# Kernel tuning notes

Hardware: AMD Instinct MI355X
Metric: run time of the kernel (lower is better)

Reference implementation:

```python
import jax, jax.numpy as jnp
import numpy as np

HEAD_DIM = 128
SCALE = 1.0 / np.sqrt(HEAD_DIM)  # standard 1/sqrt(d) attention scaling


def setup_inputs() -> dict:
    key = jax.random.key(0)
    kq, kk, kv = jax.random.split(key, 3)
    q = jax.random.normal(kq, (2, 32, 2048, HEAD_DIM), dtype=jnp.float16)
    k = jax.random.normal(kk, (2, 8, 2048, HEAD_DIM), dtype=jnp.float16)
    v = jax.random.normal(kv, (2, 8, 2048, HEAD_DIM), dtype=jnp.float16)
    return {"q": q, "k": k, "v": v}


def reference(q, k, v):
    # GQA attention: each of the g = H // KVH query heads in a group attends
    # against the group's single shared K/V head (no K/V duplication).
    b, h, sq, d = q.shape
    kvh = k.shape[1]
    g = h // kvh
    # [b, kvh, g, sq, d] -- group-packed Q, mirroring the kernel's _pack_q
    qg = q.reshape(b, kvh, g, sq, d)
    # fp32 accumulation as in flash-attention kernels
    scores = jnp.einsum(
        'bhgqd,bhkd->bhgqk',
        qg.astype(jnp.float32), k.astype(jnp.float32)) * SCALE
    p = jax.nn.softmax(scores, axis=-1)  # non-causal, full attention
    o = jnp.einsum('bhgqk,bhkd->bhgqd', p, v.astype(jnp.float32))
    return o.reshape(b, h, sq, d).astype(q.dtype)
```

## Files before the change

### kernel.cpp

```cpp
#include <hip/hip_runtime.h>

#define SEQ   2048
#define HD    128
#define BN    64
#define NITER (SEQ / BN)

typedef __fp16 f16x8  __attribute__((ext_vector_type(8)));
typedef float  f32x4  __attribute__((ext_vector_type(4)));
typedef float  f32x16 __attribute__((ext_vector_type(16)));

__device__ __forceinline__ unsigned pkh(float a, float b) {
  auto h = __builtin_amdgcn_cvt_pkrtz(a, b);
  return __builtin_bit_cast(unsigned, h);
}

__global__ __launch_bounds__(256, 2)
void fa_gqa_kernel(const float* __restrict__ Q,
                   const float* __restrict__ K,
                   const float* __restrict__ V,
                   float* __restrict__ O)
{
  __shared__ unsigned short kt_lds[64 * HD];
  __shared__ unsigned short vt_lds[HD * 64];

  const int tid  = threadIdx.x;
  const int lane = tid & 63;
  const int w    = tid >> 6;
  const int ml   = lane & 31;
  const int hi   = lane >> 5;
  const bool hib = (hi != 0);

  const int F     = blockIdx.x;
  const int xcd   = F & 7;
  const int s     = F >> 3;
  const int bh    = xcd * 8 + (s >> 4);
  const int qtile = s & 15;

  const int b = bh >> 5;
  const int h = bh & 31;
  const long qrow0 = (long)bh * SEQ + qtile * 128 + w * 32;
  const float* Qw = Q + qrow0 * HD;
  float*       Ow = O + qrow0 * HD;
  const long kvoff = (long)(b * 8 + (h >> 2)) * SEQ * HD;
  const float* Kb = K + kvoff;
  const float* Vb = V + kvoff;

  f16x8 qf[8];
#pragma unroll
  for (int dc = 0; dc < 8; ++dc) {
    const float4* qp = (const float4*)(Qw + ml * HD + dc * 16 + hi * 8);
    float4 a = qp[0], bq = qp[1];
    int4 t;
    t.x = (int)pkh(a.x, a.y);
    t.y = (int)pkh(a.z, a.w);
    t.z = (int)pkh(bq.x, bq.y);
    t.w = (int)pkh(bq.z, bq.w);
    qf[dc] = __builtin_bit_cast(f16x8, t);
  }

  f32x16 oacc[4];
#pragma unroll
  for (int dt = 0; dt < 4; ++dt)
    oacc[dt] = (f32x16)(0.f);

  float mst = -1e30f;
  float lst = 0.f;

  const float K1 = 0.08838834764831845f * 1.4426950408889634f;

  const int krow = tid >> 2;
  const int kq4  = tid & 3;
  const int kq   = tid >> 4;
  const int dc8  = tid & 15;

  for (int it = 0; it < NITER; ++it) {
    const int k0 = it * BN;

    const float* kp = Kb + (long)(k0 + krow) * HD + kq4 * 32;
    int4 ks[4];
#pragma unroll
    for (int jj = 0; jj < 4; ++jj) {
      float4 e = ((const float4*)kp)[2 * jj];
      float4 o = ((const float4*)kp)[2 * jj + 1];
      ks[jj].x = (int)pkh(e.x, e.y);
      ks[jj].y = (int)pkh(e.z, e.w);
      ks[jj].z = (int)pkh(o.x, o.y);
      ks[jj].w = (int)pkh(o.z, o.w);
    }

    const float* vp = Vb + (long)(k0 + 4 * kq) * HD + dc8 * 8;
    float4 vr[4][2];
#pragma unroll
    for (int r = 0; r < 4; ++r) {
      vr[r][0] = ((const float4*)(vp + r * HD))[0];
      vr[r][1] = ((const float4*)(vp + r * HD))[1];
    }
    uint2 vs[8];
#pragma unroll
    for (int jd = 0; jd < 8; ++jd) {
      const int hsel = jd >> 2, e = jd & 3;
      float x0 = ((const float*)&vr[0][hsel])[e];
      float x1 = ((const float*)&vr[1][hsel])[e];
      float x2 = ((const float*)&vr[2][hsel])[e];
      float x3 = ((const float*)&vr[3][hsel])[e];
      vs[jd].x = pkh(x0, x1);
      vs[jd].y = pkh(x2, x3);
    }

    __syncthreads();

#pragma unroll
    for (int jj = 0; jj < 4; ++jj) {
      int j = kq4 * 4 + jj;
      int pos = j ^ (krow & 15);
      *(int4*)(kt_lds + krow * HD + pos * 8) = ks[jj];
    }
#pragma unroll
    for (int jd = 0; jd < 8; ++jd) {
      int d = dc8 * 8 + jd;
      int sw3 = ((d >> 3) ^ d) & 7;
      int pos = (kq >> 1) ^ sw3;
      *(uint2*)(vt_lds + d * 64 + pos * 8 + (kq & 1) * 4) = vs[jd];
    }

    __syncthreads();

    f32x16 sacc[2];
    sacc[0] = (f32x16)(0.f);
    sacc[1] = (f32x16)(0.f);

    __builtin_amdgcn_s_setprio(1);
#pragma unroll
    for (int dc = 0; dc < 8; ++dc) {
#pragma unroll
      for (int kt = 0; kt < 2; ++kt) {
        int row = kt * 32 + ml;
        int pos = (2 * dc + hi) ^ (row & 15);
        f16x8 af = *(const f16x8*)(kt_lds + row * HD + pos * 8);
        sacc[kt] = __builtin_amdgcn_mfma_f32_32x32x16_f16(
            af, qf[dc], sacc[kt], 0, 0, 0);
      }
    }
    __builtin_amdgcn_s_setprio(0);

    float x0 = fmaxf(sacc[0][0], sacc[1][0]);
    float x1 = fmaxf(sacc[0][1], sacc[1][1]);
    float x2 = fmaxf(sacc[0][2], sacc[1][2]);
    float x3 = fmaxf(sacc[0][3], sacc[1][3]);
#pragma unroll
    for (int r = 4; r < 16; r += 4) {
      x0 = fmaxf(x0, fmaxf(sacc[0][r + 0], sacc[1][r + 0]));
      x1 = fmaxf(x1, fmaxf(sacc[0][r + 1], sacc[1][r + 1]));
      x2 = fmaxf(x2, fmaxf(sacc[0][r + 2], sacc[1][r + 2]));
      x3 = fmaxf(x3, fmaxf(sacc[0][r + 3], sacc[1][r + 3]));
    }
    float mx = fmaxf(fmaxf(x0, x1), fmaxf(x2, x3));
    mx = fmaxf(mx, __shfl_xor(mx, 32, 64));

    if (__any(mx > mst)) {
      float mnew = fmaxf(mst, mx);
      float alpha = __builtin_amdgcn_exp2f(K1 * (mst - mnew));
      mst = mnew;
      lst *= alpha;
#pragma unroll
      for (int dt = 0; dt < 4; ++dt)
        oacc[dt] *= alpha;
    }

    const float nm = -K1 * mst;
    float p0 = 0.f, p1 = 0.f, p2 = 0.f, p3 = 0.f;
#pragma unroll
    for (int kt = 0; kt < 2; ++kt) {
#pragma unroll
      for (int r = 0; r < 16; r += 4) {
        float e0 = __builtin_amdgcn_exp2f(fmaf(sacc[kt][r + 0], K1, nm));
        float e1 = __builtin_amdgcn_exp2f(fmaf(sacc[kt][r + 1], K1, nm));
        float e2 = __builtin_amdgcn_exp2f(fmaf(sacc[kt][r + 2], K1, nm));
        float e3 = __builtin_amdgcn_exp2f(fmaf(sacc[kt][r + 3], K1, nm));
        sacc[kt][r + 0] = e0; p0 += e0;
        sacc[kt][r + 1] = e1; p1 += e1;
        sacc[kt][r + 2] = e2; p2 += e2;
        sacc[kt][r + 3] = e3; p3 += e3;
      }
    }
    lst += (p0 + p1) + (p2 + p3);

#pragma unroll
    for (int st = 0; st < 4; ++st) {
      const int kt = st >> 1;
      const int R  = 8 * (st & 1);
      unsigned pA0 = pkh(sacc[kt][R + 0], sacc[kt][R + 1]);
      unsigned pA1 = pkh(sacc[kt][R + 2], sacc[kt][R + 3]);
      unsigned pB0 = pkh(sacc[kt][R + 4], sacc[kt][R + 5]);
      unsigned pB1 = pkh(sacc[kt][R + 6], sacc[kt][R + 7]);
      unsigned s0 = hib ? pA0 : pB0;
      unsigned s1 = hib ? pA1 : pB1;
      unsigned r0 = (unsigned)__shfl_xor((int)s0, 32, 64);
      unsigned r1 = (unsigned)__shfl_xor((int)s1, 32, 64);
      int4 bf;
      bf.x = (int)(hib ? r0 : pA0);
      bf.y = (int)(hib ? r1 : pA1);
      bf.z = (int)(hib ? pB0 : r0);
      bf.w = (int)(hib ? pB1 : r1);
      f16x8 pfrag = __builtin_bit_cast(f16x8, bf);
      __builtin_amdgcn_s_setprio(1);
#pragma unroll
      for (int dt = 0; dt < 4; ++dt) {
        int d = dt * 32 + ml;
        int pos = (2 * st + hi) ^ (((d >> 3) ^ d) & 7);
        f16x8 vf = *(const f16x8*)(vt_lds + d * 64 + pos * 8);
        oacc[dt] = __builtin_amdgcn_mfma_f32_32x32x16_f16(
            vf, pfrag, oacc[dt], 0, 0, 0);
      }
      __builtin_amdgcn_s_setprio(0);
    }
  }

  float lf = lst + __shfl_xor(lst, 32, 64);
  float linv = 1.0f / lf;
#pragma unroll
  for (int dt = 0; dt < 4; ++dt) {
#pragma unroll
    for (int t = 0; t < 4; ++t) {
      f32x4 ov;
      ov[0] = oacc[dt][4 * t + 0] * linv;
      ov[1] = oacc[dt][4 * t + 1] * linv;
      ov[2] = oacc[dt][4 * t + 2] * linv;
      ov[3] = oacc[dt][4 * t + 3] * linv;
      *(f32x4*)(Ow + ml * HD + dt * 32 + 8 * t + 4 * hi) = ov;
    }
  }
}

extern "C" void kernel_launch(void* const* d_in, const int* in_sizes, int n_in,
                              void* d_out, int out_size, void* d_ws, size_t ws_size,
                              hipStream_t stream) {
  const float* q = (const float*)d_in[0];
  const float* k = (const float*)d_in[1];
  const float* v = (const float*)d_in[2];
  float* o = (float*)d_out;
  fa_gqa_kernel<<<dim3(1024), dim3(256), 0, stream>>>(q, k, v, o);
}
```

Measured before the change: 331.1 us.

## Pre-convert K/V to swizzled fp16 tiles and double-buffer via direct global-to-LDS loads

Adds a pre-pass kernel that converts K and V from fp32 to fp16 once, writing them in the already-swizzled LDS tile layout (V transposed) into workspace. The attention kernel then copies each tile straight into a double-buffered LDS slot with global_load_lds, prefetching the next tile while the current one is computed, and drops one barrier per iteration and the setprio hints. This removes the redundant per-block fp32 loads and conversions of the shared K/V, which were repeated by every q-tile and head in a group, and halves K/V global traffic. In exchange it adds a second launch, workspace traffic and double the LDS footprint. The code shows no explicit wait on the async LDS loads (e.g. vmcnt) before the barrier, so correctness relies on the barrier or compiler-inserted waits.

```diff
diff --git a/kernel.cpp b/kernel.cpp
--- a/kernel.cpp
+++ b/kernel.cpp
@@ -1,9 +1,11 @@
 #include <hip/hip_runtime.h>
 
-#define SEQ   2048
-#define HD    128
-#define BN    64
-#define NITER (SEQ / BN)
+#define SEQ    2048
+#define HD     128
+#define BN     64
+#define NITER  (SEQ / BN)
+#define NKVH   16
+#define TILE_E 8192
 
 typedef __fp16 f16x8  __attribute__((ext_vector_type(8)));
 typedef float  f32x4  __attribute__((ext_vector_type(4)));
@@ -14,14 +16,76 @@
   return __builtin_bit_cast(unsigned, h);
 }
 
+__device__ __forceinline__ void gl_lds16(const unsigned short* g, unsigned short* l) {
+  __builtin_amdgcn_global_load_lds(
+      (const __attribute__((address_space(1))) void*)g,
+      (__attribute__((address_space(3))) void*)l, 16, 0, 0);
+}
+
+__global__ __launch_bounds__(256)
+void cvt_kv(const float* __restrict__ K, const float* __restrict__ V,
+            unsigned short* __restrict__ Kw, unsigned short* __restrict__ Vw)
+{
+  __shared__ unsigned short kt[TILE_E];
+  __shared__ unsigned short vt[TILE_E];
+  const int tid = threadIdx.x;
+  const int T   = blockIdx.x;
+  const long base = (long)T * TILE_E;
+
+  const int krow = tid >> 2, kq4 = tid & 3;
+  const float* kp = K + base + (long)krow * HD + kq4 * 32;
+#pragma unroll
+  for (int jj = 0; jj < 4; ++jj) {
+    float4 e = ((const float4*)kp)[2 * jj];
+    float4 o = ((const float4*)kp)[2 * jj + 1];
+    int4 ksj;
+    ksj.x = (int)pkh(e.x, e.y);
+    ksj.y = (int)pkh(e.z, e.w);
+    ksj.z = (int)pkh(o.x, o.y);
+    ksj.w = (int)pkh(o.z, o.w);
+    int j = kq4 * 4 + jj;
+    int pos = j ^ (krow & 15);
+    *(int4*)(kt + krow * HD + pos * 8) = ksj;
+  }
+  const int kq = tid >> 4, dc8 = tid & 15;
+  const float* vp = V + base + (long)(4 * kq) * HD + dc8 * 8;
+  float4 vr[4][2];
+#pragma unroll
+  for (int r = 0; r < 4; ++r) {
+    vr[r][0] = ((const float4*)(vp + r * HD))[0];
+    vr[r][1] = ((const float4*)(vp + r * HD))[1];
+  }
+#pragma unroll
+  for (int jd = 0; jd < 8; ++jd) {
+    const int hsel = jd >> 2, e = jd & 3;
+    uint2 v2;
+    v2.x = pkh(((const float*)&vr[0][hsel])[e], ((const float*)&vr[1][hsel])[e]);
+    v2.y = pkh(((const float*)&vr[2][hsel])[e], ((const float*)&vr[3][hsel])[e]);
+    int d = dc8 * 8 + jd;
+    int sw3 = ((d >> 3) ^ d) & 7;
+    int pos = (kq >> 1) ^ sw3;
+    *(uint2*)(vt + d * 64 + pos * 8 + (kq & 1) * 4) = v2;
+  }
+  __syncthreads();
+  int4* kd = (int4*)(Kw + (long)T * TILE_E);
+  int4* vd = (int4*)(Vw + (long)T * TILE_E);
+  const int4* ksrc = (const int4*)kt;
+  const int4* vsrc = (const int4*)vt;
+#pragma unroll
+  for (int i = 0; i < 4; ++i) {
+    kd[i * 256 + tid] = ksrc[i * 256 + tid];
+    vd[i * 256 + tid] = vsrc[i * 256 + tid];
+  }
+}
+
 __global__ __launch_bounds__(256, 2)
 void fa_gqa_kernel(const float* __restrict__ Q,
-                   const float* __restrict__ K,
-                   const float* __restrict__ V,
+                   const unsigned short* __restrict__ Kw,
+                   const unsigned short* __restrict__ Vw,
                    float* __restrict__ O)
 {
-  __shared__ unsigned short kt_lds[64 * HD];
-  __shared__ unsigned short vt_lds[HD * 64];
+  __shared__ unsigned short kt_lds[2][TILE_E];
+  __shared__ unsigned short vt_lds[2][TILE_E];
 
   const int tid  = threadIdx.x;
   const int lane = tid & 63;
@@ -41,9 +105,7 @@
   const long qrow0 = (long)bh * SEQ + qtile * 128 + w * 32;
   const float* Qw = Q + qrow0 * HD;
   float*       Ow = O + qrow0 * HD;
-  const long kvoff = (long)(b * 8 + (h >> 2)) * SEQ * HD;
-  const float* Kb = K + kvoff;
-  const float* Vb = V + kvoff;
+  const int kvh = b * 8 + (h >> 2);
 
   f16x8 qf[8];
 #pragma unroll
@@ -68,80 +130,50 @@
 
   const float K1 = 0.08838834764831845f * 1.4426950408889634f;
 
-  const int krow = tid >> 2;
-  const int kq4  = tid & 3;
-  const int kq   = tid >> 4;
-  const int dc8  = tid & 15;
+  const unsigned short* kwb = Kw + (long)kvh * NITER * TILE_E;
+  const unsigned short* vwb = Vw + (long)kvh * NITER * TILE_E;
+  const int woff = w * 2048;
+
+  {
+    const unsigned short* ks = kwb + woff + lane * 8;
+    const unsigned short* vs = vwb + woff + lane * 8;
+#pragma unroll
+    for (int c = 0; c < 4; ++c) {
+      gl_lds16(ks + c * 512, &kt_lds[0][woff + c * 512]);
+      gl_lds16(vs + c * 512, &vt_lds[0][woff + c * 512]);
+    }
+  }
 
   for (int it = 0; it < NITER; ++it) {
-    const int k0 = it * BN;
-
-    const float* kp = Kb + (long)(k0 + krow) * HD + kq4 * 32;
-    int4 ks[4];
-#pragma unroll
-    for (int jj = 0; jj < 4; ++jj) {
-      float4 e = ((const float4*)kp)[2 * jj];
-      float4 o = ((const float4*)kp)[2 * jj + 1];
-      ks[jj].x = (int)pkh(e.x, e.y);
-      ks[jj].y = (int)pkh(e.z, e.w);
-      ks[jj].z = (int)pkh(o.x, o.y);
-      ks[jj].w = (int)pkh(o.z, o.w);
-    }
-
-    const float* vp = Vb + (long)(k0 + 4 * kq) * HD + dc8 * 8;
-    float4 vr[4][2];
-#pragma unroll
-    for (int r = 0; r < 4; ++r) {
-      vr[r][0] = ((const float4*)(vp + r * HD))[0];
-      vr[r][1] = ((const float4*)(vp + r * HD))[1];
-    }
-    uint2 vs[8];
-#pragma unroll
-    for (int jd = 0; jd < 8; ++jd) {
-      const int hsel = jd >> 2, e = jd & 3;
-      float x0 = ((const float*)&vr[0][hsel])[e];
-      float x1 = ((const float*)&vr[1][hsel])[e];
-      float x2 = ((const float*)&vr[2][hsel])[e];
-      float x3 = ((const float*)&vr[3][hsel])[e];
-      vs[jd].x = pkh(x0, x1);
-      vs[jd].y = pkh(x2, x3);
-    }
-
+    const int cur = it & 1;
     __syncthreads();
 
-#pragma unroll
-    for (int jj = 0; jj < 4; ++jj) {
-      int j = kq4 * 4 + jj;
-      int pos = j ^ (krow & 15);
-      *(int4*)(kt_lds + krow * HD + pos * 8) = ks[jj];
-    }
-#pragma unroll
-    for (int jd = 0; jd < 8; ++jd) {
-      int d = dc8 * 8 + jd;
-      int sw3 = ((d >> 3) ^ d) & 7;
-      int pos = (kq >> 1) ^ sw3;
-      *(uint2*)(vt_lds + d * 64 + pos * 8 + (kq & 1) * 4) = vs[jd];
-    }
-
-    __syncthreads();
+    if (it + 1 < NITER) {
+      const unsigned short* ks = kwb + (long)(it + 1) * TILE_E + woff + lane * 8;
+      const unsigned short* vs = vwb + (long)(it + 1) * TILE_E + woff + lane * 8;
+      const int nxt = cur ^ 1;
+#pragma unroll
+      for (int c = 0; c < 4; ++c) {
+        gl_lds16(ks + c * 512, &kt_lds[nxt][woff + c * 512]);
+        gl_lds16(vs + c * 512, &vt_lds[nxt][woff + c * 512]);
+      }
+    }
 
     f32x16 sacc[2];
     sacc[0] = (f32x16)(0.f);
     sacc[1] = (f32x16)(0.f);
 
-    __builtin_amdgcn_s_setprio(1);
 #pragma unroll
     for (int dc = 0; dc < 8; ++dc) {
 #pragma unroll
       for (int kt = 0; kt < 2; ++kt) {
         int row = kt * 32 + ml;
         int pos = (2 * dc + hi) ^ (row & 15);
-        f16x8 af = *(const f16x8*)(kt_lds + row * HD + pos * 8);
+        f16x8 af = *(const f16x8*)(kt_lds[cur] + row * HD + pos * 8);
         sacc[kt] = __builtin_amdgcn_mfma_f32_32x32x16_f16(
             af, qf[dc], sacc[kt], 0, 0, 0);
       }
     }
-    __builtin_amdgcn_s_setprio(0);
 
     float x0 = fmaxf(sacc[0][0], sacc[1][0]);
     float x1 = fmaxf(sacc[0][1], sacc[1][1]);
@@ -203,16 +235,14 @@
       bf.z = (int)(hib ? pB0 : r0);
       bf.w = (int)(hib ? pB1 : r1);
       f16x8 pfrag = __builtin_bit_cast(f16x8, bf);
-      __builtin_amdgcn_s_setprio(1);
 #pragma unroll
       for (int dt = 0; dt < 4; ++dt) {
         int d = dt * 32 + ml;
         int pos = (2 * st + hi) ^ (((d >> 3) ^ d) & 7);
-        f16x8 vf = *(const f16x8*)(vt_lds + d * 64 + pos * 8);
+        f16x8 vf = *(const f16x8*)(vt_lds[cur] + d * 64 + pos * 8);
         oacc[dt] = __builtin_amdgcn_mfma_f32_32x32x16_f16(
             vf, pfrag, oacc[dt], 0, 0, 0);
       }
-      __builtin_amdgcn_s_setprio(0);
     }
   }
 
@@ -239,5 +269,8 @@
   const float* k = (const float*)d_in[1];
   const float* v = (const float*)d_in[2];
   float* o = (float*)d_out;
-  fa_gqa_kernel<<<dim3(1024), dim3(256), 0, stream>>>(q, k, v, o);
-}
+  unsigned short* Kw = (unsigned short*)d_ws;
+  unsigned short* Vw = Kw + (long)NKVH * NITER * TILE_E;
+  cvt_kv<<<dim3(NKVH * NITER), dim3(256), 0, stream>>>(k, v, Kw, Vw);
+  fa_gqa_kernel<<<dim3(1024), dim3(256), 0, stream>>>(q, Kw, Vw, o);
+}
```

After: 312.5 us, median of 2. 5.6% less time.
